# Optimization experiments

Hardware: AMD Instinct MI355X
Metric: run time of the kernel (lower is better)

Reference implementation:

```python
import jax
jax.config.update("jax_enable_x64", True)  # hashing needs true int64 like torch
import jax.numpy as jnp
import numpy as np
import itertools

N_DIM = 3
N_ENTRIES = 4194304  # 2**22
N_FEATURE = 4
BATCH = 2097152  # 2**21 sample points
GRIDS = np.array([128.0, 128.0, 128.0], dtype=np.float32)
PRIMES = np.array([1, 19349663, 83492791], dtype=np.int64)
BIT_TABLE = np.array(list(itertools.product([0, 1], repeat=N_DIM)), dtype=np.int32)  # (2^D, D)


def setup_inputs() -> dict:
    key = jax.random.key(0)
    k1, k2 = jax.random.split(key)
    position = jax.random.uniform(k1, (BATCH, N_DIM), dtype=jnp.float32)  # in [0,1)^D
    hash_table = (jax.random.uniform(k2, (N_ENTRIES, N_FEATURE), dtype=jnp.float32) - 0.5) * 2e-4
    return {"position": position, "hash_table": hash_table}


def reference(position, hash_table):
    grids = jnp.asarray(GRIDS)           # (D,) float32
    bit = jnp.asarray(BIT_TABLE)         # (2^D, D) int32
    primes = jnp.asarray(PRIMES)         # (D,) int64

    # findGrid: lower corner on the integer grid
    lower = jnp.floor(position * grids).astype(jnp.int32)          # (B, D)
    # all 2^D corners of the enclosing cell
    corner = lower[:, None, :] + bit[None, :, :]                    # (B, 2^D, D)

    # spatial hash: XOR of index*prime, reduced mod table size each step (as torch does)
    h = jnp.zeros(corner.shape[:-1], dtype=jnp.int64)               # (B, 2^D)
    for i in range(N_DIM):
        h = jnp.bitwise_xor(h, corner[..., i].astype(jnp.int64) * primes[i]) % N_ENTRIES

    corner_value = hash_table[h]                                    # (B, 2^D, F) gather

    # multilinear interpolation coefficients (faithful to source's weight assignment)
    lower_f = lower / grids                                         # (B, D)
    upper_f = (lower + 1) / grids                                   # (B, D)
    size = (upper_f - lower_f)[0]                                   # (D,) uniform cell size
    coef = jnp.stack([(position - lower_f) / size,
                      (upper_f - position) / size], axis=-1)        # (B, D, 2)
    # weight per corner = prod over dims of the bit-selected coefficient
    w = jnp.prod(coef[:, jnp.arange(N_DIM)[None, :], bit], axis=2)  # (B, 2^D)

    return jnp.sum(corner_value * w[..., None], axis=1)             # (B, F)
```

## Files before the change

### kernel.cpp

```cpp
#include <hip/hip_runtime.h>
#include <stdint.h>


#define HASH_MASK 0x3FFFFFu
#define P1 19349663u
#define P2 83492791u
#define NBUCK 64
#define CHUNKS 16
#define FB 64
#define NSUP 4096
#define PPT 16
#define K3_BLOCK 256
#define PPB (K3_BLOCK * PPT)
#define CMAX 2560

__device__ __forceinline__ uint32_t bucket_of(float px, float py, float pz) {
    uint32_t bx = ((uint32_t)(int)floorf(px * 128.0f)) >> 5;
    uint32_t by = ((uint32_t)(int)floorf(py * 128.0f)) >> 5;
    uint32_t bz = ((uint32_t)(int)floorf(pz * 128.0f)) >> 5;
    return (bx << 4) | (by << 2) | bz;
}

__device__ __forceinline__ uint32_t fine_of(float px, float py, float pz) {
    uint32_t fx = (((uint32_t)(int)floorf(px * 128.0f)) >> 3) & 3u;
    uint32_t fy = (((uint32_t)(int)floorf(py * 128.0f)) >> 3) & 3u;
    uint32_t fz = (((uint32_t)(int)floorf(pz * 128.0f)) >> 3) & 3u;
    return (fx << 4) | (fy << 2) | fz;
}

__device__ __forceinline__ float4 interp_point(float px, float py, float pz,
                                               const float* __restrict__ table) {
    int lx = (int)floorf(px * 128.0f);
    int ly = (int)floorf(py * 128.0f);
    int lz = (int)floorf(pz * 128.0f);
    const float inv = 1.0f / 128.0f;
    float w0x = (px - (float)lx * inv) * 128.0f;
    float w1x = ((float)(lx + 1) * inv - px) * 128.0f;
    float w0y = (py - (float)ly * inv) * 128.0f;
    float w1y = ((float)(ly + 1) * inv - py) * 128.0f;
    float w0z = (pz - (float)lz * inv) * 128.0f;
    float w1z = ((float)(lz + 1) * inv - pz) * 128.0f;
    uint32_t hx0 = (uint32_t)lx, hx1 = (uint32_t)(lx + 1);
    uint32_t hy0 = (uint32_t)ly * P1, hy1 = (uint32_t)(ly + 1) * P1;
    uint32_t hz0 = (uint32_t)lz * P2, hz1 = (uint32_t)(lz + 1) * P2;
    float acc0 = 0.f, acc1 = 0.f, acc2 = 0.f, acc3 = 0.f;
#pragma unroll
    for (int c = 0; c < 8; ++c) {
        int bx = (c >> 2) & 1, by = (c >> 1) & 1, bz = c & 1;
        uint32_t h = ((bx ? hx1 : hx0) ^ (by ? hy1 : hy0) ^ (bz ? hz1 : hz0)) & HASH_MASK;
        const float4 v = *reinterpret_cast<const float4*>(table + (size_t)h * 4);
        float w = ((bx ? w1x : w0x) * (by ? w1y : w0y)) * (bz ? w1z : w0z);
        acc0 += v.x * w; acc1 += v.y * w; acc2 += v.z * w; acc3 += v.w * w;
    }
    return make_float4(acc0, acc1, acc2, acc3);
}

__global__ __launch_bounds__(K3_BLOCK) void hist_kernel(
    const float* __restrict__ pos, uint32_t* __restrict__ hist, int batch)
{
    __shared__ uint32_t h[NBUCK];
    int tid = threadIdx.x;
    size_t start = (size_t)blockIdx.x * PPB;
    if (tid < NBUCK) h[tid] = 0;
    __syncthreads();
#pragma unroll
    for (int k = 0; k < PPT; ++k) {
        size_t i = start + (size_t)k * K3_BLOCK + tid;
        if (i < (size_t)batch) {
            float px = pos[3 * i + 0];
            float py = pos[3 * i + 1];
            float pz = pos[3 * i + 2];
            atomicAdd(&h[bucket_of(px, py, pz)], 1u);
        }
    }
    __syncthreads();
    if (tid < NBUCK && h[tid]) atomicAdd(&hist[tid], h[tid]);
}

__global__ __launch_bounds__(64) void scan_kernel(
    const uint32_t* __restrict__ hist, uint32_t* __restrict__ cursor)
{
    int t = threadIdx.x;
    uint32_t v = hist[t];
    uint32_t inc = v;
    for (int off = 1; off < 64; off <<= 1) {
        uint32_t n = __shfl_up(inc, off);
        if (t >= off) inc += n;
    }
    cursor[t] = inc - v;
}

__global__ __launch_bounds__(K3_BLOCK) void scatter_kernel(
    const float* __restrict__ pos, uint32_t* __restrict__ cursor,
    float4* __restrict__ sorted, uint8_t* __restrict__ key, int batch)
{
    __shared__ float4 staged[PPB];
    __shared__ uint32_t h[NBUCK], lbase[NBUCK], gbase[NBUCK], lcur[NBUCK];
    int tid = threadIdx.x;
    size_t start = (size_t)blockIdx.x * PPB;

    if (tid < NBUCK) h[tid] = 0;
    __syncthreads();

    float px[PPT], py[PPT], pz[PPT];
    uint32_t bb[PPT];
#pragma unroll
    for (int k = 0; k < PPT; ++k) {
        size_t i = start + (size_t)k * K3_BLOCK + tid;
        px[k] = pos[3 * i + 0];
        py[k] = pos[3 * i + 1];
        pz[k] = pos[3 * i + 2];
        bb[k] = bucket_of(px[k], py[k], pz[k]);
        atomicAdd(&h[bb[k]], 1u);
    }
    __syncthreads();

    if (tid < NBUCK) {
        uint32_t v = h[tid];
        uint32_t inc = v;
        for (int off = 1; off < 64; off <<= 1) {
            uint32_t n = __shfl_up(inc, off);
            if (tid >= off) inc += n;
        }
        uint32_t excl = inc - v;
        lbase[tid] = excl;
        lcur[tid] = excl;
        gbase[tid] = atomicAdd(&cursor[tid], v);
    }
    __syncthreads();

#pragma unroll
    for (int k = 0; k < PPT; ++k) {
        size_t i = start + (size_t)k * K3_BLOCK + tid;
        uint32_t slot = atomicAdd(&lcur[bb[k]], 1u);
        staged[slot] = make_float4(px[k], py[k], pz[k], __uint_as_float((uint32_t)i));
    }
    __syncthreads();

#pragma unroll
    for (int k = 0; k < PPT; ++k) {
        int j = k * K3_BLOCK + tid;
        float4 s = staged[j];
        uint32_t b = bucket_of(s.x, s.y, s.z);
        uint32_t slot = gbase[b] + ((uint32_t)j - lbase[b]);
        sorted[slot] = s;
        key[slot] = (uint8_t)fine_of(s.x, s.y, s.z);
    }
}

__global__ __launch_bounds__(256) void fineA_kernel(
    const uint8_t* __restrict__ key, const uint32_t* __restrict__ cursor,
    uint32_t* __restrict__ chist)
{
    __shared__ uint32_t h[FB];
    int tid = threadIdx.x;
    int b = blockIdx.x >> 4, c = blockIdx.x & (CHUNKS - 1);
    uint32_t bs = b ? cursor[b - 1] : 0u;
    uint32_t be = cursor[b];
    uint32_t n = be - bs;
    uint32_t csz = (n + CHUNKS - 1) / CHUNKS;
    uint32_t cs = bs + (uint32_t)c * csz;
    uint32_t ce = min(cs + csz, be);

    if (tid < FB) h[tid] = 0;
    __syncthreads();
    for (uint32_t j = cs + tid; j < ce; j += 256)
        atomicAdd(&h[key[j]], 1u);
    __syncthreads();
    if (tid < FB) chist[((uint32_t)blockIdx.x << 6) + tid] = h[tid];
}

__global__ __launch_bounds__(64) void fineB_kernel(
    const uint32_t* __restrict__ chist, const uint32_t* __restrict__ cursor,
    uint32_t* __restrict__ cbase, uint32_t* __restrict__ sstart)
{
    int b = blockIdx.x;
    int f = threadIdx.x;
    uint32_t bs = b ? cursor[b - 1] : 0u;

    uint32_t cnt[CHUNKS];
    uint32_t tot = 0;
#pragma unroll
    for (int c = 0; c < CHUNKS; ++c) {
        cnt[c] = chist[(((uint32_t)b * CHUNKS + c) << 6) + f];
        tot += cnt[c];
    }
    uint32_t inc = tot;
    for (int off = 1; off < 64; off <<= 1) {
        uint32_t n = __shfl_up(inc, off);
        if (f >= off) inc += n;
    }
    uint32_t fbase = bs + inc - tot;
    sstart[((uint32_t)b << 6) + f] = fbase;
    uint32_t run = fbase;
#pragma unroll
    for (int c = 0; c < CHUNKS; ++c) {
        cbase[(((uint32_t)b * CHUNKS + c) << 6) + f] = run;
        run += cnt[c];
    }
}

__global__ __launch_bounds__(256) void fineC_kernel(
    const float4* __restrict__ sorted, const uint8_t* __restrict__ key,
    const uint32_t* __restrict__ cursor, const uint32_t* __restrict__ chist,
    const uint32_t* __restrict__ cbase, float4* __restrict__ sorted2)
{
    __shared__ float4 staged[CMAX];
    __shared__ uint32_t lbase[FB], lcur[FB], gb[FB];
    int tid = threadIdx.x;
    int b = blockIdx.x >> 4, c = blockIdx.x & (CHUNKS - 1);
    uint32_t bs = b ? cursor[b - 1] : 0u;
    uint32_t be = cursor[b];
    uint32_t n = be - bs;
    uint32_t csz = (n + CHUNKS - 1) / CHUNKS;
    uint32_t cs = bs + (uint32_t)c * csz;
    uint32_t ce = min(cs + csz, be);
    if (ce <= cs) return;
    uint32_t m = ce - cs;

    if (tid < FB) {
        uint32_t v = chist[(((uint32_t)b * CHUNKS + c) << 6) + tid];
        uint32_t inc = v;
        for (int off = 1; off < 64; off <<= 1) {
            uint32_t nn = __shfl_up(inc, off);
            if (tid >= off) inc += nn;
        }
        lbase[tid] = inc - v;
        lcur[tid] = inc - v;
        gb[tid] = cbase[(((uint32_t)b * CHUNKS + c) << 6) + tid];
    }
    __syncthreads();

    for (uint32_t j = cs + tid; j < ce; j += 256) {
        float4 s = sorted[j];
        uint32_t slot = atomicAdd(&lcur[key[j]], 1u);
        staged[slot] = s;
    }
    __syncthreads();

    for (uint32_t j = tid; j < m; j += 256) {
        float4 s = staged[j];
        uint32_t f = fine_of(s.x, s.y, s.z);
        sorted2[gb[f] + (j - lbase[f])] = s;
    }
}

__global__ __launch_bounds__(256) void interp_super_kernel(
    const float4* __restrict__ sorted2, const uint32_t* __restrict__ sstart,
    const float* __restrict__ table, float4* __restrict__ out4, int batch)
{
    __shared__ float4 corners[729];
    int bid = blockIdx.x;
    int swz = (bid & 7) * (NSUP >> 3) + (bid >> 3);
    int tid = threadIdx.x;
    uint32_t r = (uint32_t)swz;
    uint32_t start = sstart[r];
    uint32_t end = (r == NSUP - 1) ? (uint32_t)batch : sstart[r + 1];
    if (start >= end) return;

    float4 s0 = sorted2[start];
    int rbx = (((int)floorf(s0.x * 128.0f)) >> 3) << 3;
    int rby = (((int)floorf(s0.y * 128.0f)) >> 3) << 3;
    int rbz = (((int)floorf(s0.z * 128.0f)) >> 3) << 3;

    for (int idx = tid; idx < 729; idx += 256) {
        int ci = idx / 81;
        int rem = idx - ci * 81;
        int cj = rem / 9;
        int ck = rem - cj * 9;
        uint32_t h = ((uint32_t)(rbx + ci) ^
                      (uint32_t)(rby + cj) * P1 ^
                      (uint32_t)(rbz + ck) * P2) & HASH_MASK;
        corners[idx] = *reinterpret_cast<const float4*>(table + (size_t)h * 4);
    }
    __syncthreads();

    const float inv = 1.0f / 128.0f;
    for (uint32_t p = start + tid; p < end; p += 256) {
        float4 s = sorted2[p];
        float px = s.x, py = s.y, pz = s.z;
        int lx = (int)floorf(px * 128.0f);
        int ly = (int)floorf(py * 128.0f);
        int lz = (int)floorf(pz * 128.0f);
        float w0x = (px - (float)lx * inv) * 128.0f;
        float w1x = ((float)(lx + 1) * inv - px) * 128.0f;
        float w0y = (py - (float)ly * inv) * 128.0f;
        float w1y = ((float)(ly + 1) * inv - py) * 128.0f;
        float w0z = (pz - (float)lz * inv) * 128.0f;
        float w1z = ((float)(lz + 1) * inv - pz) * 128.0f;
        int li = lx - rbx, lj = ly - rby, lk = lz - rbz;
        int base = li * 81 + lj * 9 + lk;

        float acc0 = 0.f, acc1 = 0.f, acc2 = 0.f, acc3 = 0.f;
#pragma unroll
        for (int c = 0; c < 8; ++c) {
            int bx = (c >> 2) & 1, by = (c >> 1) & 1, bz = c & 1;
            float4 v = corners[base + bx * 81 + by * 9 + bz];
            float w = ((bx ? w1x : w0x) * (by ? w1y : w0y)) * (bz ? w1z : w0z);
            acc0 += v.x * w; acc1 += v.y * w; acc2 += v.z * w; acc3 += v.w * w;
        }
        out4[__float_as_uint(s.w)] = make_float4(acc0, acc1, acc2, acc3);
    }
}

__global__ __launch_bounds__(256) void interp_direct_kernel(
    const float* __restrict__ pos, const float* __restrict__ table,
    float4* __restrict__ out4, int batch)
{
    int i = blockIdx.x * 256 + threadIdx.x;
    if (i >= batch) return;
    out4[i] = interp_point(pos[3 * (size_t)i], pos[3 * (size_t)i + 1],
                           pos[3 * (size_t)i + 2], table);
}

extern "C" void kernel_launch(void* const* d_in, const int* in_sizes, int n_in,
                              void* d_out, int out_size, void* d_ws, size_t ws_size,
                              hipStream_t stream) {
    const float* pos   = (const float*)d_in[0];
    const float* table = (const float*)d_in[1];
    float4* out4 = (float4*)d_out;

    int batch = in_sizes[0] / 3;
    int blocks256 = (batch + 255) / 256;

    size_t sorted_off  = 512;
    size_t sorted2_off = sorted_off + (size_t)batch * 16;
    size_t chist_off   = sorted2_off + (size_t)batch * 16;
    size_t chist_bytes = (size_t)NBUCK * CHUNKS * FB * 4;
    size_t cbase_off   = chist_off + chist_bytes;
    size_t sstart_off  = cbase_off + chist_bytes;
    size_t key_off     = sstart_off + (size_t)NSUP * 4;
    size_t need_full   = key_off + (size_t)batch;

    bool exact = (batch % PPB == 0) && ((blocks256 & 7) == 0);
    if (ws_size < need_full || !exact) {
        interp_direct_kernel<<<blocks256, 256, 0, stream>>>(pos, table, out4, batch);
        return;
    }

    uint32_t* hist    = (uint32_t*)d_ws;
    uint32_t* cursor  = (uint32_t*)((char*)d_ws + 256);
    float4*   sorted  = (float4*)((char*)d_ws + sorted_off);
    float4*   sorted2 = (float4*)((char*)d_ws + sorted2_off);
    uint32_t* chist   = (uint32_t*)((char*)d_ws + chist_off);
    uint32_t* cbase   = (uint32_t*)((char*)d_ws + cbase_off);
    uint32_t* sstart  = (uint32_t*)((char*)d_ws + sstart_off);
    uint8_t*  key     = (uint8_t*)((char*)d_ws + key_off);

    int sblocks = batch / PPB;

    hipMemsetAsync(hist, 0, NBUCK * sizeof(uint32_t), stream);
    hist_kernel<<<sblocks, K3_BLOCK, 0, stream>>>(pos, hist, batch);
    scan_kernel<<<1, 64, 0, stream>>>(hist, cursor);
    scatter_kernel<<<sblocks, K3_BLOCK, 0, stream>>>(pos, cursor, sorted, key, batch);
    fineA_kernel<<<NBUCK * CHUNKS, 256, 0, stream>>>(key, cursor, chist);
    fineB_kernel<<<NBUCK, 64, 0, stream>>>(chist, cursor, cbase, sstart);
    fineC_kernel<<<NBUCK * CHUNKS, 256, 0, stream>>>(sorted, key, cursor, chist,
                                                     cbase, sorted2);
    interp_super_kernel<<<NSUP, 256, 0, stream>>>(sorted2, sstart, table, out4, batch);
}
```

Measured before the change: 106.9 us.

## Coarsen fine binning to 16^3 superblocks with 1024-thread interp blocks

Fine sub-bucketing changes from 64 sub-cells of 8^3 to 8 sub-cells of 16^3 per coarse bucket. The interpolation kernel now caches a 17^3 corner tile (about 78KB LDS) per superblock in 1024-thread blocks, which cuts redundant halo table gathers (4913 vs 8*729 corners). The superblock origin is now derived from the block index instead of being read from the first point. The fine histogram gets per-wave LDS copies to reduce atomic contention. The cost is large LDS use limiting occupancy and fewer, larger interpolation blocks (512).

```diff
diff --git a/kernel.cpp b/kernel.cpp
--- a/kernel.cpp
+++ b/kernel.cpp
@@ -7,8 +7,9 @@
 #define P2 83492791u
 #define NBUCK 64
 #define CHUNKS 16
-#define FB 64
-#define NSUP 4096
+#define FB 8
+#define NSUP 512
+#define NCORN 4913
 #define PPT 16
 #define K3_BLOCK 256
 #define PPB (K3_BLOCK * PPT)
@@ -22,10 +23,10 @@
 }
 
 __device__ __forceinline__ uint32_t fine_of(float px, float py, float pz) {
-    uint32_t fx = (((uint32_t)(int)floorf(px * 128.0f)) >> 3) & 3u;
-    uint32_t fy = (((uint32_t)(int)floorf(py * 128.0f)) >> 3) & 3u;
-    uint32_t fz = (((uint32_t)(int)floorf(pz * 128.0f)) >> 3) & 3u;
-    return (fx << 4) | (fy << 2) | fz;
+    uint32_t fx = (((uint32_t)(int)floorf(px * 128.0f)) >> 4) & 1u;
+    uint32_t fy = (((uint32_t)(int)floorf(py * 128.0f)) >> 4) & 1u;
+    uint32_t fz = (((uint32_t)(int)floorf(pz * 128.0f)) >> 4) & 1u;
+    return (fx << 2) | (fy << 1) | fz;
 }
 
 __device__ __forceinline__ float4 interp_point(float px, float py, float pz,
@@ -152,8 +153,9 @@
     const uint8_t* __restrict__ key, const uint32_t* __restrict__ cursor,
     uint32_t* __restrict__ chist)
 {
-    __shared__ uint32_t h[FB];
-    int tid = threadIdx.x;
+    __shared__ uint32_t h[4][FB];
+    int tid = threadIdx.x;
+    int wave = tid >> 6;
     int b = blockIdx.x >> 4, c = blockIdx.x & (CHUNKS - 1);
     uint32_t bs = b ? cursor[b - 1] : 0u;
     uint32_t be = cursor[b];
@@ -162,12 +164,14 @@
     uint32_t cs = bs + (uint32_t)c * csz;
     uint32_t ce = min(cs + csz, be);
 
-    if (tid < FB) h[tid] = 0;
+    if (tid < 4 * FB) h[tid >> 3][tid & 7] = 0;
     __syncthreads();
     for (uint32_t j = cs + tid; j < ce; j += 256)
-        atomicAdd(&h[key[j]], 1u);
-    __syncthreads();
-    if (tid < FB) chist[((uint32_t)blockIdx.x << 6) + tid] = h[tid];
+        atomicAdd(&h[wave][key[j]], 1u);
+    __syncthreads();
+    if (tid < FB)
+        chist[((uint32_t)blockIdx.x << 3) + tid] =
+            h[0][tid] + h[1][tid] + h[2][tid] + h[3][tid];
 }
 
 __global__ __launch_bounds__(64) void fineB_kernel(
@@ -180,23 +184,27 @@
 
     uint32_t cnt[CHUNKS];
     uint32_t tot = 0;
-#pragma unroll
-    for (int c = 0; c < CHUNKS; ++c) {
-        cnt[c] = chist[(((uint32_t)b * CHUNKS + c) << 6) + f];
-        tot += cnt[c];
+    if (f < FB) {
+#pragma unroll
+        for (int c = 0; c < CHUNKS; ++c) {
+            cnt[c] = chist[(((uint32_t)b * CHUNKS + c) << 3) + f];
+            tot += cnt[c];
+        }
     }
     uint32_t inc = tot;
-    for (int off = 1; off < 64; off <<= 1) {
+    for (int off = 1; off < FB; off <<= 1) {
         uint32_t n = __shfl_up(inc, off);
         if (f >= off) inc += n;
     }
-    uint32_t fbase = bs + inc - tot;
-    sstart[((uint32_t)b << 6) + f] = fbase;
-    uint32_t run = fbase;
-#pragma unroll
-    for (int c = 0; c < CHUNKS; ++c) {
-        cbase[(((uint32_t)b * CHUNKS + c) << 6) + f] = run;
-        run += cnt[c];
+    if (f < FB) {
+        uint32_t fbase = bs + inc - tot;
+        sstart[((uint32_t)b << 3) + f] = fbase;
+        uint32_t run = fbase;
+#pragma unroll
+        for (int c = 0; c < CHUNKS; ++c) {
+            cbase[(((uint32_t)b * CHUNKS + c) << 3) + f] = run;
+            run += cnt[c];
+        }
     }
 }
 
@@ -219,15 +227,15 @@
     uint32_t m = ce - cs;
 
     if (tid < FB) {
-        uint32_t v = chist[(((uint32_t)b * CHUNKS + c) << 6) + tid];
+        uint32_t v = chist[(((uint32_t)b * CHUNKS + c) << 3) + tid];
         uint32_t inc = v;
-        for (int off = 1; off < 64; off <<= 1) {
+        for (int off = 1; off < FB; off <<= 1) {
             uint32_t nn = __shfl_up(inc, off);
             if (tid >= off) inc += nn;
         }
         lbase[tid] = inc - v;
         lcur[tid] = inc - v;
-        gb[tid] = cbase[(((uint32_t)b * CHUNKS + c) << 6) + tid];
+        gb[tid] = cbase[(((uint32_t)b * CHUNKS + c) << 3) + tid];
     }
     __syncthreads();
 
@@ -245,11 +253,11 @@
     }
 }
 
-__global__ __launch_bounds__(256) void interp_super_kernel(
+__global__ __launch_bounds__(1024) void interp_super16_kernel(
     const float4* __restrict__ sorted2, const uint32_t* __restrict__ sstart,
     const float* __restrict__ table, float4* __restrict__ out4, int batch)
 {
-    __shared__ float4 corners[729];
+    __shared__ float4 corners[NCORN];
     int bid = blockIdx.x;
     int swz = (bid & 7) * (NSUP >> 3) + (bid >> 3);
     int tid = threadIdx.x;
@@ -258,16 +266,16 @@
     uint32_t end = (r == NSUP - 1) ? (uint32_t)batch : sstart[r + 1];
     if (start >= end) return;
 
-    float4 s0 = sorted2[start];
-    int rbx = (((int)floorf(s0.x * 128.0f)) >> 3) << 3;
-    int rby = (((int)floorf(s0.y * 128.0f)) >> 3) << 3;
-    int rbz = (((int)floorf(s0.z * 128.0f)) >> 3) << 3;
-
-    for (int idx = tid; idx < 729; idx += 256) {
-        int ci = idx / 81;
-        int rem = idx - ci * 81;
-        int cj = rem / 9;
-        int ck = rem - cj * 9;
+    uint32_t b = r >> 3, f = r & 7u;
+    int rbx = (int)((((b >> 4) & 3u) << 5) | (((f >> 2) & 1u) << 4));
+    int rby = (int)((((b >> 2) & 3u) << 5) | (((f >> 1) & 1u) << 4));
+    int rbz = (int)(((b & 3u) << 5) | ((f & 1u) << 4));
+
+    for (int idx = tid; idx < NCORN; idx += 1024) {
+        int ci = idx / 289;
+        int rem = idx - ci * 289;
+        int cj = rem / 17;
+        int ck = rem - cj * 17;
         uint32_t h = ((uint32_t)(rbx + ci) ^
                       (uint32_t)(rby + cj) * P1 ^
                       (uint32_t)(rbz + ck) * P2) & HASH_MASK;
@@ -276,7 +284,7 @@
     __syncthreads();
 
     const float inv = 1.0f / 128.0f;
-    for (uint32_t p = start + tid; p < end; p += 256) {
+    for (uint32_t p = start + tid; p < end; p += 1024) {
         float4 s = sorted2[p];
         float px = s.x, py = s.y, pz = s.z;
         int lx = (int)floorf(px * 128.0f);
@@ -289,13 +297,13 @@
         float w0z = (pz - (float)lz * inv) * 128.0f;
         float w1z = ((float)(lz + 1) * inv - pz) * 128.0f;
         int li = lx - rbx, lj = ly - rby, lk = lz - rbz;
-        int base = li * 81 + lj * 9 + lk;
+        int cb = li * 289 + lj * 17 + lk;
 
         float acc0 = 0.f, acc1 = 0.f, acc2 = 0.f, acc3 = 0.f;
 #pragma unroll
-        for (int c = 0; c < 8; ++c) {
-            int bx = (c >> 2) & 1, by = (c >> 1) & 1, bz = c & 1;
-            float4 v = corners[base + bx * 81 + by * 9 + bz];
+        for (int c8 = 0; c8 < 8; ++c8) {
+            int bx = (c8 >> 2) & 1, by = (c8 >> 1) & 1, bz = c8 & 1;
+            float4 v = corners[cb + bx * 289 + by * 17 + bz];
             float w = ((bx ? w1x : w0x) * (by ? w1y : w0y)) * (bz ? w1z : w0z);
             acc0 += v.x * w; acc1 += v.y * w; acc2 += v.z * w; acc3 += v.w * w;
         }
@@ -357,5 +365,6 @@
     fineB_kernel<<<NBUCK, 64, 0, stream>>>(chist, cursor, cbase, sstart);
     fineC_kernel<<<NBUCK * CHUNKS, 256, 0, stream>>>(sorted, key, cursor, chist,
                                                      cbase, sorted2);
-    interp_super_kernel<<<NSUP, 256, 0, stream>>>(sorted2, sstart, table, out4, batch);
-}
+    interp_super16_kernel<<<NSUP, 1024, 0, stream>>>(sorted2, sstart, table,
+                                                     out4, batch);
+}
```

Measured after the change: 109.0 us. No clear change (+1.9%).

## Enlarge interpolation supercells to 16^3 with 1024-thread blocks

Applied to the files above, without the earlier changes.

Reorders the fine key so eight 8^3 sub-cells sharing a 16^3 region sit next to each other, then processes each 16^3 region in one 1024-thread block with a 17^3 shared-memory corner cache. The aim is to cut redundant halo gathers from the hash table (729 corners per 512 cells becomes 4913 per 4096 cells) and reduce the block count. In exchange the shared memory per block grows to about 78KB, which may lower occupancy, and the corner load and sync phase is longer per block.

```diff
diff --git a/kernel.cpp b/kernel.cpp
--- a/kernel.cpp
+++ b/kernel.cpp
@@ -8,7 +8,8 @@
 #define NBUCK 64
 #define CHUNKS 16
 #define FB 64
-#define NSUP 4096
+#define NSUP16 512
+#define NCORN 4913
 #define PPT 16
 #define K3_BLOCK 256
 #define PPB (K3_BLOCK * PPT)
@@ -25,7 +26,8 @@
     uint32_t fx = (((uint32_t)(int)floorf(px * 128.0f)) >> 3) & 3u;
     uint32_t fy = (((uint32_t)(int)floorf(py * 128.0f)) >> 3) & 3u;
     uint32_t fz = (((uint32_t)(int)floorf(pz * 128.0f)) >> 3) & 3u;
-    return (fx << 4) | (fy << 2) | fz;
+    return ((fx & 1u) << 2) | ((fy & 1u) << 1) | (fz & 1u) |
+           ((fx & 2u) << 4) | ((fy & 2u) << 3) | ((fz & 2u) << 2);
 }
 
 __device__ __forceinline__ float4 interp_point(float px, float py, float pz,
@@ -245,29 +247,29 @@
     }
 }
 
-__global__ __launch_bounds__(256) void interp_super_kernel(
+__global__ __launch_bounds__(1024) void interp_super16_kernel(
     const float4* __restrict__ sorted2, const uint32_t* __restrict__ sstart,
     const float* __restrict__ table, float4* __restrict__ out4, int batch)
 {
-    __shared__ float4 corners[729];
+    __shared__ float4 corners[NCORN];
     int bid = blockIdx.x;
-    int swz = (bid & 7) * (NSUP >> 3) + (bid >> 3);
+    int swz = (bid & 7) * (NSUP16 >> 3) + (bid >> 3);
     int tid = threadIdx.x;
     uint32_t r = (uint32_t)swz;
-    uint32_t start = sstart[r];
-    uint32_t end = (r == NSUP - 1) ? (uint32_t)batch : sstart[r + 1];
+    uint32_t start = sstart[r << 3];
+    uint32_t end = (r == NSUP16 - 1) ? (uint32_t)batch : sstart[(r + 1) << 3];
     if (start >= end) return;
 
-    float4 s0 = sorted2[start];
-    int rbx = (((int)floorf(s0.x * 128.0f)) >> 3) << 3;
-    int rby = (((int)floorf(s0.y * 128.0f)) >> 3) << 3;
-    int rbz = (((int)floorf(s0.z * 128.0f)) >> 3) << 3;
-
-    for (int idx = tid; idx < 729; idx += 256) {
-        int ci = idx / 81;
-        int rem = idx - ci * 81;
-        int cj = rem / 9;
-        int ck = rem - cj * 9;
+    uint32_t b = r >> 3, g = r & 7u;
+    int rbx = (int)((((b >> 4) & 3u) << 5) | (((g >> 2) & 1u) << 4));
+    int rby = (int)((((b >> 2) & 3u) << 5) | (((g >> 1) & 1u) << 4));
+    int rbz = (int)(((b & 3u) << 5) | ((g & 1u) << 4));
+
+    for (int idx = tid; idx < NCORN; idx += 1024) {
+        int ci = idx / 289;
+        int rem = idx - ci * 289;
+        int cj = rem / 17;
+        int ck = rem - cj * 17;
         uint32_t h = ((uint32_t)(rbx + ci) ^
                       (uint32_t)(rby + cj) * P1 ^
                       (uint32_t)(rbz + ck) * P2) & HASH_MASK;
@@ -276,7 +278,7 @@
     __syncthreads();
 
     const float inv = 1.0f / 128.0f;
-    for (uint32_t p = start + tid; p < end; p += 256) {
+    for (uint32_t p = start + tid; p < end; p += 1024) {
         float4 s = sorted2[p];
         float px = s.x, py = s.y, pz = s.z;
         int lx = (int)floorf(px * 128.0f);
@@ -289,13 +291,13 @@
         float w0z = (pz - (float)lz * inv) * 128.0f;
         float w1z = ((float)(lz + 1) * inv - pz) * 128.0f;
         int li = lx - rbx, lj = ly - rby, lk = lz - rbz;
-        int base = li * 81 + lj * 9 + lk;
+        int cb = li * 289 + lj * 17 + lk;
 
         float acc0 = 0.f, acc1 = 0.f, acc2 = 0.f, acc3 = 0.f;
 #pragma unroll
-        for (int c = 0; c < 8; ++c) {
-            int bx = (c >> 2) & 1, by = (c >> 1) & 1, bz = c & 1;
-            float4 v = corners[base + bx * 81 + by * 9 + bz];
+        for (int c8 = 0; c8 < 8; ++c8) {
+            int bx = (c8 >> 2) & 1, by = (c8 >> 1) & 1, bz = c8 & 1;
+            float4 v = corners[cb + bx * 289 + by * 17 + bz];
             float w = ((bx ? w1x : w0x) * (by ? w1y : w0y)) * (bz ? w1z : w0z);
             acc0 += v.x * w; acc1 += v.y * w; acc2 += v.z * w; acc3 += v.w * w;
         }
@@ -329,7 +331,7 @@
     size_t chist_bytes = (size_t)NBUCK * CHUNKS * FB * 4;
     size_t cbase_off   = chist_off + chist_bytes;
     size_t sstart_off  = cbase_off + chist_bytes;
-    size_t key_off     = sstart_off + (size_t)NSUP * 4;
+    size_t key_off     = sstart_off + (size_t)NBUCK * FB * 4;
     size_t need_full   = key_off + (size_t)batch;
 
     bool exact = (batch % PPB == 0) && ((blocks256 & 7) == 0);
@@ -357,5 +359,6 @@
     fineB_kernel<<<NBUCK, 64, 0, stream>>>(chist, cursor, cbase, sstart);
     fineC_kernel<<<NBUCK * CHUNKS, 256, 0, stream>>>(sorted, key, cursor, chist,
                                                      cbase, sorted2);
-    interp_super_kernel<<<NSUP, 256, 0, stream>>>(sorted2, sstart, table, out4, batch);
-}
+    interp_super16_kernel<<<NSUP16, 1024, 0, stream>>>(sorted2, sstart, table,
+                                                       out4, batch);
+}
```

After: 109.9 us. 2.8% more time.
